# Performance work log

Measured on AMD Instinct MI355X. Metric: run time of the kernel, lower is better.

## Reference

```python
import jax, jax.numpy as jnp
import numpy as np

N, C = 20000, 512          # num_nodes, in_channels
E_RAND = 140000            # random edges (plus N self loops appended)
B, D = 128, 2              # num_bundles, bundle_dim
T = C // (B * D)           # feature cols per bundle (=2)
GNN_DIM = 512
NBP = B * (D * (D - 1) // 2)  # num_bun_params = 128 (1 angle per bundle since D=2)
MAX_DEG = 4
TAU = 1.0
EPS = 1e-5                 # BatchNorm1d eps


def setup_inputs() -> dict:
    key = jax.random.key(0)
    ks = jax.random.split(key, 8)
    x = jax.random.normal(ks[0], (N, C), jnp.float32)
    # edges: random + self-loops so every node has positive out-degree (finite deg_inv)
    src = jax.random.randint(ks[1], (E_RAND,), 0, N)
    dst = jax.random.randint(ks[2], (E_RAND,), 0, N)
    loop = jnp.arange(N)
    edge_index = jnp.stack([jnp.concatenate([src, loop]),
                            jnp.concatenate([dst, loop])]).astype(jnp.int64)
    s = 0.02
    W1 = jax.random.normal(ks[3], (C, GNN_DIM), jnp.float32) * s   # struct_enc lin1
    b1 = jnp.zeros((GNN_DIM,), jnp.float32)
    W2 = jax.random.normal(ks[4], (GNN_DIM, NBP), jnp.float32) * s # struct_enc lin2
    b2 = jnp.zeros((NBP,), jnp.float32)
    Wlin = jax.random.normal(ks[5], (C, C), jnp.float32) * s       # BuNNConv.lin
    blin = jnp.zeros((C,), jnp.float32)
    gamma = jnp.ones((C,), jnp.float32)                            # BatchNorm weight
    beta = jnp.zeros((C,), jnp.float32)                            # BatchNorm bias
    return dict(x=x, W1=W1, b1=b1, W2=W2, b2=b2, Wlin=Wlin, blin=blin,
                gamma=gamma, beta=beta, edge_index=edge_index)


def reference(x, W1, b1, W2, b2, Wlin, blin, gamma, beta, edge_index):
    src, dst = edge_index[0], edge_index[1]
    # degree of edge_index[0]; edge_weight = deg_inv[row] with row = edge_index[1]
    deg = jax.ops.segment_sum(jnp.ones_like(src, jnp.float32), src, num_segments=N)
    ew = (1.0 / deg)[dst]                                   # [E]

    # struct encoder (num_gnn == 0 branch): Linear -> GELU -> Linear -> 1 angle/bundle
    theta = jax.nn.gelu(x @ W1 + b1, approximate=False) @ W2 + b2   # [N, B]
    c, s = jnp.cos(theta), jnp.sin(theta)
    R = jnp.stack([jnp.stack([c, -s], -1),
                   jnp.stack([s, c], -1)], -2)              # [N, B, 2, 2] orthogonal

    # map into bundle frame
    vf = x.reshape(N, B, D, T)
    vf = jnp.einsum('nbij,nbjt->nbit', R, vf)
    h = vf.reshape(N, C)

    # truncated heat-kernel diffusion via scatter message passing
    cur = h
    for k in range(1, MAX_DEG + 1):
        agg = jax.ops.segment_sum(ew[:, None] * cur[src], dst, num_segments=N)
        cur = (-TAU / k) * (cur - agg)
        h = h + cur

    h = h @ Wlin + blin

    # map back with R^T
    vf = h.reshape(N, B, D, T)
    vf = jnp.einsum('nbji,nbjt->nbit', R, vf)
    h = vf.reshape(N, C)

    h = x + h                                # residual (dropout p = 0.0)
    mean = h.mean(axis=0)                    # BatchNorm1d, training mode, biased var
    var = h.var(axis=0)
    return (h - mean) / jnp.sqrt(var + EPS) * gamma + beta
```

## Files before the change

kernel.cpp:

```cpp
#include <hip/hip_runtime.h>

#define CC   512
#define BB_  128
#define BM 64
#define BN 128
#define BK 32

typedef __attribute__((ext_vector_type(8))) short short8;
typedef __attribute__((ext_vector_type(8))) unsigned short u16x8;
typedef __attribute__((ext_vector_type(4))) float f32x4;
typedef __attribute__((ext_vector_type(2))) float f32x2;
typedef __attribute__((ext_vector_type(4))) unsigned short u16x4;

__device__ __forceinline__ unsigned short f2bf(float f) {
  union { float f; unsigned u; } v; v.f = f;
  return (unsigned short)((v.u + 0x7FFFu + ((v.u >> 16) & 1u)) >> 16);
}
__device__ __forceinline__ float bf2f(unsigned short b) {
  union { unsigned u; float f; } v; v.u = ((unsigned)b) << 16;
  return v.f;
}

__device__ __forceinline__ void gload_lds16(const unsigned short* g, unsigned short* l) {
  __builtin_amdgcn_global_load_lds(
      (const __attribute__((address_space(1))) void*)g,
      (__attribute__((address_space(3))) void*)l, 16, 0, 0);
}

__global__ void k_zero(int* __restrict__ a, int* __restrict__ b, int* __restrict__ c,
                       float* __restrict__ d, float* __restrict__ e, int n) {
  int i = blockIdx.x * blockDim.x + threadIdx.x;
  if (i < n) { a[i] = 0; b[i] = 0; c[i] = 0; }
  if (i < CC) { d[i] = 0.f; e[i] = 0.f; }
}

__global__ void k_count(const int* __restrict__ src, const int* __restrict__ dst,
                        int* __restrict__ cnt_src, int* __restrict__ cnt_dst, int E) {
  int e = blockIdx.x * blockDim.x + threadIdx.x;
  if (e < E) {
    atomicAdd(&cnt_src[src[e]], 1);
    atomicAdd(&cnt_dst[dst[e]], 1);
  }
}

__global__ __launch_bounds__(1024) void k_scan(const int* __restrict__ cnt,
                                               const int* __restrict__ cnt_src,
                                               int* __restrict__ rp,
                                               float* __restrict__ dinv, int n) {
  __shared__ int sm[1024];
  int tid = threadIdx.x;
  for (int i = tid; i < n; i += 1024) dinv[i] = 1.0f / (float)cnt_src[i];
  int chunk = (n + 1023) >> 10;
  int beg = tid * chunk;
  int end = beg + chunk; if (end > n) end = n;
  int s = 0;
  for (int i = beg; i < end && i < n; ++i) s += cnt[i];
  sm[tid] = s;
  __syncthreads();
  for (int off = 1; off < 1024; off <<= 1) {
    int v = (tid >= off) ? sm[tid - off] : 0;
    __syncthreads();
    sm[tid] += v;
    __syncthreads();
  }
  int run = (tid == 0) ? 0 : sm[tid - 1];
  for (int i = beg; i < end && i < n; ++i) { rp[i] = run; run += cnt[i]; }
  if (tid == 0) rp[n] = sm[1023];
}

__global__ void k_fill(const int* __restrict__ src, const int* __restrict__ dst,
                       const int* __restrict__ rp, int* __restrict__ fil,
                       int* __restrict__ col, int E) {
  int e = blockIdx.x * blockDim.x + threadIdx.x;
  if (e < E) {
    int d = dst[e];
    int p = atomicAdd(&fil[d], 1);
    col[rp[d] + p] = src[e];
  }
}

__global__ void k_conv_bf16(const float* __restrict__ in, unsigned short* __restrict__ out,
                            int validRows, int total4) {
  int i4 = blockIdx.x * blockDim.x + threadIdx.x;
  if (i4 >= total4) return;
  int row = i4 / (CC / 4);
  u16x4 o;
  if (row < validRows) {
    f32x4 v = ((const f32x4*)in)[i4];
    o[0] = f2bf(v[0]); o[1] = f2bf(v[1]); o[2] = f2bf(v[2]); o[3] = f2bf(v[3]);
  } else {
    o[0] = 0; o[1] = 0; o[2] = 0; o[3] = 0;
  }
  ((u16x4*)out)[i4] = o;
}

__global__ void k_transconv(const float* __restrict__ W, unsigned short* __restrict__ Wt,
                            int K, int Nw) {
  __shared__ float tile[32][33];
  int n0 = blockIdx.x * 32, k0 = blockIdx.y * 32;
  int tx = threadIdx.x, ty = threadIdx.y;
  for (int j = 0; j < 4; ++j)
    tile[ty + j * 8][tx] = W[(k0 + ty + j * 8) * Nw + n0 + tx];
  __syncthreads();
  for (int j = 0; j < 4; ++j)
    Wt[(n0 + ty + j * 8) * K + k0 + tx] = f2bf(tile[tx][ty + j * 8]);
}

template <int EPI>
__device__ __forceinline__ void epi_store(float v, int row, int colL, void* outp,
                                          const float* x, unsigned short* c0,
                                          int Nw, int nvalid) {
  if (EPI == 0) {
    ((float*)outp)[(size_t)row * Nw + colL] = v;
  } else if (EPI == 1) {
    float g = 0.5f * v * (1.0f + erff(v * 0.70710678118654752f));
    ((unsigned short*)outp)[(size_t)row * Nw + colL] = f2bf(g);
  } else {
    size_t bidx = (size_t)row * Nw + colL;
    if (row < nvalid) {
      float sv, cv;
      sincosf(v, &sv, &cv);
      f32x2 o; o[0] = cv; o[1] = sv;
      ((f32x2*)outp)[bidx] = o;
      f32x4 xv = ((const f32x4*)x)[bidx];
      u16x4 rr;
      rr[0] = f2bf(cv * xv[0] - sv * xv[2]);
      rr[1] = f2bf(cv * xv[1] - sv * xv[3]);
      rr[2] = f2bf(sv * xv[0] + cv * xv[2]);
      rr[3] = f2bf(sv * xv[1] + cv * xv[3]);
      ((u16x4*)c0)[bidx] = rr;
    } else {
      u16x4 rr; rr[0] = 0; rr[1] = 0; rr[2] = 0; rr[3] = 0;
      ((u16x4*)c0)[bidx] = rr;
    }
  }
}

template <int EPI>
__global__ __launch_bounds__(256) void k_gemm(const unsigned short* __restrict__ A,
                                              const unsigned short* __restrict__ Bt,
                                              const float* __restrict__ bias,
                                              void* __restrict__ outp,
                                              const float* __restrict__ x,
                                              unsigned short* __restrict__ c0,
                                              int K, int Nw, int nvalid) {
  __shared__ unsigned short As[2][BM * BK];
  __shared__ unsigned short Bs[2][BN * BK];
  const int m0 = blockIdx.x * BM;
  const int n0 = blockIdx.y * BN;
  const int tid = threadIdx.x;
  const int wid = tid >> 6, lane = tid & 63;
  const int wr = wid >> 1, wc = wid & 1;
  const int l15 = lane & 15, kg = lane >> 4;
  const int arow = wid * 16 + (lane >> 2);
  const int aseg = (lane & 3) * 8;

  f32x4 acc00 = {}, acc01 = {}, acc02 = {}, acc03 = {};
  f32x4 acc10 = {}, acc11 = {}, acc12 = {}, acc13 = {};

  const int nt = K / BK;
  gload_lds16(&A[(size_t)(m0 + arow) * K + aseg],       &As[0][wid * 512]);
  gload_lds16(&Bt[(size_t)(n0 + arow) * K + aseg],      &Bs[0][wid * 512]);
  gload_lds16(&Bt[(size_t)(n0 + 64 + arow) * K + aseg], &Bs[0][2048 + wid * 512]);
  __syncthreads();

  for (int kk = 0; kk < nt; ++kk) {
    const int cur = kk & 1;
    if (kk + 1 < nt) {
      const int kt = (kk + 1) * BK;
      gload_lds16(&A[(size_t)(m0 + arow) * K + kt + aseg],       &As[cur ^ 1][wid * 512]);
      gload_lds16(&Bt[(size_t)(n0 + arow) * K + kt + aseg],      &Bs[cur ^ 1][wid * 512]);
      gload_lds16(&Bt[(size_t)(n0 + 64 + arow) * K + kt + aseg], &Bs[cur ^ 1][2048 + wid * 512]);
    }
    short8 af0 = *(const short8*)&As[cur][(wr * 32 +  0 + l15) * BK + kg * 8];
    short8 af1 = *(const short8*)&As[cur][(wr * 32 + 16 + l15) * BK + kg * 8];
    short8 bg0 = *(const short8*)&Bs[cur][(wc * 64 +  0 + l15) * BK + kg * 8];
    short8 bg1 = *(const short8*)&Bs[cur][(wc * 64 + 16 + l15) * BK + kg * 8];
    short8 bg2 = *(const short8*)&Bs[cur][(wc * 64 + 32 + l15) * BK + kg * 8];
    short8 bg3 = *(const short8*)&Bs[cur][(wc * 64 + 48 + l15) * BK + kg * 8];
    acc00 = __builtin_amdgcn_mfma_f32_16x16x32_bf16(af0, bg0, acc00, 0, 0, 0);
    acc01 = __builtin_amdgcn_mfma_f32_16x16x32_bf16(af0, bg1, acc01, 0, 0, 0);
    acc02 = __builtin_amdgcn_mfma_f32_16x16x32_bf16(af0, bg2, acc02, 0, 0, 0);
    acc03 = __builtin_amdgcn_mfma_f32_16x16x32_bf16(af0, bg3, acc03, 0, 0, 0);
    acc10 = __builtin_amdgcn_mfma_f32_16x16x32_bf16(af1, bg0, acc10, 0, 0, 0);
    acc11 = __builtin_amdgcn_mfma_f32_16x16x32_bf16(af1, bg1, acc11, 0, 0, 0);
    acc12 = __builtin_amdgcn_mfma_f32_16x16x32_bf16(af1, bg2, acc12, 0, 0, 0);
    acc13 = __builtin_amdgcn_mfma_f32_16x16x32_bf16(af1, bg3, acc13, 0, 0, 0);
    __syncthreads();
  }

#define DO_EPI(ACC, MI, NI)                                                     \
  do {                                                                          \
    const int row_ = m0 + wr * 32 + (MI) * 16 + kg * 4;                         \
    const int col_ = n0 + wc * 64 + (NI) * 16 + l15;                            \
    const float b_ = bias[col_];                                                \
    epi_store<EPI>(ACC[0] + b_, row_ + 0, col_, outp, x, c0, Nw, nvalid);       \
    epi_store<EPI>(ACC[1] + b_, row_ + 1, col_, outp, x, c0, Nw, nvalid);       \
    epi_store<EPI>(ACC[2] + b_, row_ + 2, col_, outp, x, c0, Nw, nvalid);       \
    epi_store<EPI>(ACC[3] + b_, row_ + 3, col_, outp, x, c0, Nw, nvalid);       \
  } while (0)

  DO_EPI(acc00, 0, 0); DO_EPI(acc01, 0, 1); DO_EPI(acc02, 0, 2); DO_EPI(acc03, 0, 3);
  DO_EPI(acc10, 1, 0); DO_EPI(acc11, 1, 1); DO_EPI(acc12, 1, 2); DO_EPI(acc13, 1, 3);
#undef DO_EPI
}

__global__ __launch_bounds__(256) void k_diffuse(const unsigned short* __restrict__ cur,
                                                 unsigned short* __restrict__ nxt,
                                                 const float* __restrict__ dinv,
                                                 const int* __restrict__ rp,
                                                 const int* __restrict__ col,
                                                 float coef, int n) {
  int w = threadIdx.x >> 6, lane = threadIdx.x & 63;
  int v = blockIdx.x * 4 + w;
  if (v >= n) return;
  int beg = rp[v], end = rp[v + 1];
  const u16x8* curv = (const u16x8*)cur;
  float s[8] = {0.f,0.f,0.f,0.f,0.f,0.f,0.f,0.f};
  for (int e = beg; e < end; ++e) {
    int u = col[e];
    u16x8 r = curv[(size_t)u * 64 + lane];
    #pragma unroll
    for (int j = 0; j < 8; ++j) s[j] += bf2f(r[j]);
  }
  float di = dinv[v];
  u16x8 cv = curv[(size_t)v * 64 + lane];
  u16x8 o;
  #pragma unroll
  for (int j = 0; j < 8; ++j) o[j] = f2bf((bf2f(cv[j]) - s[j] * di) * coef);
  ((u16x8*)nxt)[(size_t)v * 64 + lane] = o;
}

__global__ __launch_bounds__(256) void k_diffuse_final(const unsigned short* __restrict__ c0,
                                                       const unsigned short* __restrict__ c1,
                                                       const unsigned short* __restrict__ c2,
                                                       const unsigned short* __restrict__ cur,
                                                       unsigned short* __restrict__ hb,
                                                       const float* __restrict__ dinv,
                                                       const int* __restrict__ rp,
                                                       const int* __restrict__ col,
                                                       float coef, int n) {
  int w = threadIdx.x >> 6, lane = threadIdx.x & 63;
  int v = blockIdx.x * 4 + w;
  if (v >= n) return;
  int beg = rp[v], end = rp[v + 1];
  const u16x8* curv = (const u16x8*)cur;
  float s[8] = {0.f,0.f,0.f,0.f,0.f,0.f,0.f,0.f};
  for (int e = beg; e < end; ++e) {
    int u = col[e];
    u16x8 r = curv[(size_t)u * 64 + lane];
    #pragma unroll
    for (int j = 0; j < 8; ++j) s[j] += bf2f(r[j]);
  }
  float di = dinv[v];
  size_t o = (size_t)v * 64 + lane;
  u16x8 cv = curv[o];
  u16x8 a0 = ((const u16x8*)c0)[o];
  u16x8 a1 = ((const u16x8*)c1)[o];
  u16x8 a2 = ((const u16x8*)c2)[o];
  u16x8 hv;
  #pragma unroll
  for (int j = 0; j < 8; ++j) {
    float c3v = bf2f(cv[j]);
    float c4v = (c3v - s[j] * di) * coef;
    hv[j] = f2bf(bf2f(a0[j]) + bf2f(a1[j]) + bf2f(a2[j]) + c3v + c4v);
  }
  ((u16x8*)hb)[o] = hv;
}

__global__ __launch_bounds__(256) void k_rotback_stats(const float* __restrict__ x,
                                                       const f32x2* __restrict__ cs,
                                                       const float* __restrict__ h2,
                                                       float* __restrict__ out,
                                                       float* __restrict__ colsum,
                                                       float* __restrict__ colsq,
                                                       int nb) {
  __shared__ float ssum[CC], ssq[CC];
  int t = threadIdx.x;
  for (int c = t; c < CC; c += 256) { ssum[c] = 0.f; ssq[c] = 0.f; }
  __syncthreads();
  int cg = ((blockIdx.x << 8) + t) & (BB_ - 1);
  float ls0 = 0.f, ls1 = 0.f, ls2 = 0.f, ls3 = 0.f;
  float lq0 = 0.f, lq1 = 0.f, lq2 = 0.f, lq3 = 0.f;
  for (int idx = (blockIdx.x << 8) + t; idx < nb; idx += gridDim.x << 8) {
    f32x2 a = cs[idx];
    float c = a[0], s = a[1];
    f32x4 v = ((const f32x4*)h2)[idx];
    f32x4 xx = ((const f32x4*)x)[idx];
    f32x4 o;
    o[0] = xx[0] + c * v[0] + s * v[2];
    o[1] = xx[1] + c * v[1] + s * v[3];
    o[2] = xx[2] - s * v[0] + c * v[2];
    o[3] = xx[3] - s * v[1] + c * v[3];
    ((f32x4*)out)[idx] = o;
    ls0 += o[0]; lq0 += o[0] * o[0];
    ls1 += o[1]; lq1 += o[1] * o[1];
    ls2 += o[2]; lq2 += o[2] * o[2];
    ls3 += o[3]; lq3 += o[3] * o[3];
  }
  atomicAdd(&ssum[cg * 4 + 0], ls0); atomicAdd(&ssq[cg * 4 + 0], lq0);
  atomicAdd(&ssum[cg * 4 + 1], ls1); atomicAdd(&ssq[cg * 4 + 1], lq1);
  atomicAdd(&ssum[cg * 4 + 2], ls2); atomicAdd(&ssq[cg * 4 + 2], lq2);
  atomicAdd(&ssum[cg * 4 + 3], ls3); atomicAdd(&ssq[cg * 4 + 3], lq3);
  __syncthreads();
  for (int c = t; c < CC; c += 256) {
    atomicAdd(&colsum[c], ssum[c]);
    atomicAdd(&colsq[c], ssq[c]);
  }
}

__global__ void k_bnfinal(const float* __restrict__ sum, const float* __restrict__ sumsq,
                          const float* __restrict__ gamma, const float* __restrict__ beta,
                          float* __restrict__ scale, float* __restrict__ shift, int n) {
  int c = threadIdx.x;
  float inv = 1.0f / (float)n;
  float mean = sum[c] * inv;
  float var = sumsq[c] * inv - mean * mean;
  float sc = gamma[c] * rsqrtf(var + 1e-5f);
  scale[c] = sc;
  shift[c] = beta[c] - mean * sc;
}

__global__ void k_norm(float* __restrict__ out, const float* __restrict__ scale,
                       const float* __restrict__ shift, int n4) {
  int i = blockIdx.x * blockDim.x + threadIdx.x;
  if (i >= n4) return;
  int c4 = i & (CC / 4 - 1);
  f32x4 v = ((f32x4*)out)[i];
  f32x4 sc = ((const f32x4*)scale)[c4];
  f32x4 sh = ((const f32x4*)shift)[c4];
  ((f32x4*)out)[i] = v * sc + sh;
}

extern "C" void kernel_launch(void* const* d_in, const int* in_sizes, int n_in,
                              void* d_out, int out_size, void* d_ws, size_t ws_size,
                              hipStream_t stream) {
  (void)n_in; (void)out_size; (void)ws_size;
  const float* x    = (const float*)d_in[0];
  const float* W1   = (const float*)d_in[1];
  const float* b1   = (const float*)d_in[2];
  const float* W2   = (const float*)d_in[3];
  const float* b2   = (const float*)d_in[4];
  const float* Wlin = (const float*)d_in[5];
  const float* blin = (const float*)d_in[6];
  const float* gamma = (const float*)d_in[7];
  const float* beta  = (const float*)d_in[8];
  const int*   ei    = (const int*)d_in[9];

  const int n   = in_sizes[0] / CC;
  const int E   = in_sizes[9] / 2;
  const int GNN = in_sizes[2];
  const int NBP = in_sizes[4];
  const int* src = ei;
  const int* dst = ei + E;
  const int mt64 = (n + BM - 1) / BM;
  const int mpad = 20096;
  const size_t SB = (size_t)mpad * CC;

  char* ws = (char*)d_ws;
  size_t off = 0;
  auto alloc = [&](size_t bytes) -> void* {
    void* p = ws + off;
    off = (off + bytes + 255) & ~(size_t)255;
    return p;
  };
  int*   cnt_src = (int*)alloc((size_t)n * 4);
  int*   cnt_dst = (int*)alloc((size_t)n * 4);
  int*   fil     = (int*)alloc((size_t)n * 4);
  int*   rp      = (int*)alloc((size_t)(n + 1) * 4);
  int*   colx    = (int*)alloc((size_t)E * 4);
  float* dinv    = (float*)alloc((size_t)n * 4);
  float* colsum  = (float*)alloc(CC * 4);
  float* colsq   = (float*)alloc(CC * 4);
  float* scale   = (float*)alloc(CC * 4);
  float* shift   = (float*)alloc(CC * 4);
  unsigned short* W1t = (unsigned short*)alloc((size_t)GNN * CC * 2);
  unsigned short* W2t = (unsigned short*)alloc((size_t)NBP * GNN * 2);
  unsigned short* Wlt = (unsigned short*)alloc((size_t)CC * CC * 2);
  f32x2* cs = (f32x2*)alloc((size_t)mpad * BB_ * 8);
  unsigned short* c0   = (unsigned short*)alloc(SB * 2);
  unsigned short* c1   = (unsigned short*)alloc(SB * 2);
  unsigned short* slab = (unsigned short*)alloc(SB * 2 * 3);
  unsigned short* c2 = slab;
  unsigned short* c3 = slab + SB;
  unsigned short* hb = slab + 2 * SB;
  unsigned short* xb = c0;
  unsigned short* G  = c1;
  float* OUT3 = (float*)slab;

  k_zero<<<(n + 255) / 256, 256, 0, stream>>>(cnt_src, cnt_dst, fil, colsum, colsq, n);

  k_count<<<(E + 255) / 256, 256, 0, stream>>>(src, dst, cnt_src, cnt_dst, E);
  k_scan<<<1, 1024, 0, stream>>>(cnt_dst, cnt_src, rp, dinv, n);
  k_fill<<<(E + 255) / 256, 256, 0, stream>>>(src, dst, rp, fil, colx, E);

  int total4 = mpad * (CC / 4);
  k_conv_bf16<<<(total4 + 255) / 256, 256, 0, stream>>>(x, xb, n, total4);
  dim3 tb(32, 8);
  k_transconv<<<dim3(GNN / 32, CC / 32), tb, 0, stream>>>(W1, W1t, CC, GNN);
  k_transconv<<<dim3(NBP / 32, GNN / 32), tb, 0, stream>>>(W2, W2t, GNN, NBP);
  k_transconv<<<dim3(CC / 32, CC / 32), tb, 0, stream>>>(Wlin, Wlt, CC, CC);

  k_gemm<1><<<dim3(mt64, GNN / BN), 256, 0, stream>>>(xb, W1t, b1, (void*)G, nullptr, nullptr, CC, GNN, n);
  k_gemm<2><<<dim3(mt64, NBP / BN), 256, 0, stream>>>(G, W2t, b2, (void*)cs, x, c0, GNN, NBP, n);

  float coef1 = -1.0f, coef2 = -0.5f, coef3 = -1.0f / 3.0f, coef4 = -0.25f;
  k_diffuse<<<(n + 3) / 4, 256, 0, stream>>>(c0, c1, dinv, rp, colx, coef1, n);
  k_diffuse<<<(n + 3) / 4, 256, 0, stream>>>(c1, c2, dinv, rp, colx, coef2, n);
  k_diffuse<<<(n + 3) / 4, 256, 0, stream>>>(c2, c3, dinv, rp, colx, coef3, n);
  k_diffuse_final<<<(n + 3) / 4, 256, 0, stream>>>(c0, c1, c2, c3, hb, dinv, rp, colx, coef4, n);

  k_gemm<0><<<dim3(mt64, CC / BN), 256, 0, stream>>>(hb, Wlt, blin, (void*)OUT3, nullptr, nullptr, CC, CC, n);

  int nb = n * BB_;
  k_rotback_stats<<<512, 256, 0, stream>>>(x, cs, OUT3, (float*)d_out, colsum, colsq, nb);
  k_bnfinal<<<1, 512, 0, stream>>>(colsum, colsq, gamma, beta, scale, shift, n);
  k_norm<<<(nb + 255) / 256, 256, 0, stream>>>((float*)d_out, scale, shift, nb);
}
```

Baseline: 330.6 us.

## Merge diffusion passes into one cooperative kernel and fold small launches

```diff
diff --git a/kernel.cpp b/kernel.cpp
--- a/kernel.cpp
+++ b/kernel.cpp
@@ -1,4 +1,7 @@
 #include <hip/hip_runtime.h>
+#include <hip/hip_cooperative_groups.h>
+
+namespace cg = cooperative_groups;
 
 #define CC   512
 #define BB_  128
@@ -44,12 +47,9 @@
 }
 
 __global__ __launch_bounds__(1024) void k_scan(const int* __restrict__ cnt,
-                                               const int* __restrict__ cnt_src,
-                                               int* __restrict__ rp,
-                                               float* __restrict__ dinv, int n) {
+                                               int* __restrict__ rp, int n) {
   __shared__ int sm[1024];
   int tid = threadIdx.x;
-  for (int i = tid; i < n; i += 1024) dinv[i] = 1.0f / (float)cnt_src[i];
   int chunk = (n + 1023) >> 10;
   int beg = tid * chunk;
   int end = beg + chunk; if (end > n) end = n;
@@ -94,8 +94,14 @@
   ((u16x4*)out)[i4] = o;
 }
 
-__global__ void k_transconv(const float* __restrict__ W, unsigned short* __restrict__ Wt,
-                            int K, int Nw) {
+__global__ void k_transconv_all(const float* __restrict__ W1, const float* __restrict__ W2,
+                                const float* __restrict__ Wlin,
+                                unsigned short* __restrict__ W1t, unsigned short* __restrict__ W2t,
+                                unsigned short* __restrict__ Wlt) {
+  const float* W; unsigned short* Wt; int K, Nw;
+  if (blockIdx.z == 0)      { W = W1;   Wt = W1t; K = 512; Nw = 512; }
+  else if (blockIdx.z == 1) { W = W2;   Wt = W2t; K = 512; Nw = 128; if (blockIdx.x >= 4) return; }
+  else                      { W = Wlin; Wt = Wlt; K = 512; Nw = 512; }
   __shared__ float tile[32][33];
   int n0 = blockIdx.x * 32, k0 = blockIdx.y * 32;
   int tx = threadIdx.x, ty = threadIdx.y;
@@ -205,67 +211,71 @@
 #undef DO_EPI
 }
 
-__global__ __launch_bounds__(256) void k_diffuse(const unsigned short* __restrict__ cur,
-                                                 unsigned short* __restrict__ nxt,
-                                                 const float* __restrict__ dinv,
-                                                 const int* __restrict__ rp,
-                                                 const int* __restrict__ col,
-                                                 float coef, int n) {
-  int w = threadIdx.x >> 6, lane = threadIdx.x & 63;
-  int v = blockIdx.x * 4 + w;
-  if (v >= n) return;
-  int beg = rp[v], end = rp[v + 1];
-  const u16x8* curv = (const u16x8*)cur;
-  float s[8] = {0.f,0.f,0.f,0.f,0.f,0.f,0.f,0.f};
-  for (int e = beg; e < end; ++e) {
-    int u = col[e];
-    u16x8 r = curv[(size_t)u * 64 + lane];
+__global__ __launch_bounds__(256) void k_diffuse_all(const unsigned short* __restrict__ c0,
+                                                     unsigned short* __restrict__ c1,
+                                                     unsigned short* __restrict__ c2,
+                                                     unsigned short* __restrict__ c3,
+                                                     unsigned short* __restrict__ hb,
+                                                     const int* __restrict__ cnt_src,
+                                                     const int* __restrict__ rp,
+                                                     const int* __restrict__ col,
+                                                     int n) {
+  cg::grid_group grid = cg::this_grid();
+  const int nw = (gridDim.x * 256) >> 6;
+  const int w = (blockIdx.x * 256 + threadIdx.x) >> 6;
+  const int lane = threadIdx.x & 63;
+
+#define DIFF_PASS(SRC, DST, COEF)                                              \
+  for (int v = w; v < n; v += nw) {                                            \
+    int beg = rp[v], end = rp[v + 1];                                          \
+    const u16x8* curv = (const u16x8*)(SRC);                                   \
+    float s[8] = {0.f,0.f,0.f,0.f,0.f,0.f,0.f,0.f};                            \
+    for (int e = beg; e < end; ++e) {                                          \
+      int u = col[e];                                                          \
+      u16x8 r = curv[(size_t)u * 64 + lane];                                   \
+      _Pragma("unroll")                                                        \
+      for (int j = 0; j < 8; ++j) s[j] += bf2f(r[j]);                          \
+    }                                                                          \
+    float di = 1.0f / (float)cnt_src[v];                                       \
+    size_t o = (size_t)v * 64 + lane;                                          \
+    u16x8 cv = curv[o];                                                        \
+    u16x8 ov;                                                                  \
+    _Pragma("unroll")                                                          \
+    for (int j = 0; j < 8; ++j) ov[j] = f2bf((bf2f(cv[j]) - s[j] * di) * (COEF)); \
+    ((u16x8*)(DST))[o] = ov;                                                   \
+  }                                                                            \
+  grid.sync();
+
+  DIFF_PASS(c0, c1, -1.0f)
+  DIFF_PASS(c1, c2, -0.5f)
+  DIFF_PASS(c2, c3, -(1.0f / 3.0f))
+#undef DIFF_PASS
+
+  for (int v = w; v < n; v += nw) {
+    int beg = rp[v], end = rp[v + 1];
+    const u16x8* curv = (const u16x8*)c3;
+    float s[8] = {0.f,0.f,0.f,0.f,0.f,0.f,0.f,0.f};
+    for (int e = beg; e < end; ++e) {
+      int u = col[e];
+      u16x8 r = curv[(size_t)u * 64 + lane];
+      #pragma unroll
+      for (int j = 0; j < 8; ++j) s[j] += bf2f(r[j]);
+    }
+    float di = 1.0f / (float)cnt_src[v];
+    size_t o = (size_t)v * 64 + lane;
+    u16x8 cv = curv[o];
+    u16x8 a0 = ((const u16x8*)c0)[o];
+    u16x8 a1 = ((const u16x8*)c1)[o];
+    u16x8 a2 = ((const u16x8*)c2)[o];
+    u16x8 hv;
     #pragma unroll
-    for (int j = 0; j < 8; ++j) s[j] += bf2f(r[j]);
-  }
-  float di = dinv[v];
-  u16x8 cv = curv[(size_t)v * 64 + lane];
-  u16x8 o;
-  #pragma unroll
-  for (int j = 0; j < 8; ++j) o[j] = f2bf((bf2f(cv[j]) - s[j] * di) * coef);
-  ((u16x8*)nxt)[(size_t)v * 64 + lane] = o;
-}
-
-__global__ __launch_bounds__(256) void k_diffuse_final(const unsigned short* __restrict__ c0,
-                                                       const unsigned short* __restrict__ c1,
-                                                       const unsigned short* __restrict__ c2,
-                                                       const unsigned short* __restrict__ cur,
-                                                       unsigned short* __restrict__ hb,
-                                                       const float* __restrict__ dinv,
-                                                       const int* __restrict__ rp,
-                                                       const int* __restrict__ col,
-                                                       float coef, int n) {
-  int w = threadIdx.x >> 6, lane = threadIdx.x & 63;
-  int v = blockIdx.x * 4 + w;
-  if (v >= n) return;
-  int beg = rp[v], end = rp[v + 1];
-  const u16x8* curv = (const u16x8*)cur;
-  float s[8] = {0.f,0.f,0.f,0.f,0.f,0.f,0.f,0.f};
-  for (int e = beg; e < end; ++e) {
-    int u = col[e];
-    u16x8 r = curv[(size_t)u * 64 + lane];
-    #pragma unroll
-    for (int j = 0; j < 8; ++j) s[j] += bf2f(r[j]);
-  }
-  float di = dinv[v];
-  size_t o = (size_t)v * 64 + lane;
-  u16x8 cv = curv[o];
-  u16x8 a0 = ((const u16x8*)c0)[o];
-  u16x8 a1 = ((const u16x8*)c1)[o];
-  u16x8 a2 = ((const u16x8*)c2)[o];
-  u16x8 hv;
-  #pragma unroll
-  for (int j = 0; j < 8; ++j) {
-    float c3v = bf2f(cv[j]);
-    float c4v = (c3v - s[j] * di) * coef;
-    hv[j] = f2bf(bf2f(a0[j]) + bf2f(a1[j]) + bf2f(a2[j]) + c3v + c4v);
-  }
-  ((u16x8*)hb)[o] = hv;
+    for (int j = 0; j < 8; ++j) {
+      float c3v = bf2f(cv[j]);
+      float c4v = (c3v - s[j] * di) * -0.25f;
+      hv[j] = f2bf(bf2f(a0[j]) + bf2f(a1[j]) + bf2f(a2[j]) + c3v + c4v);
+    }
+    ((u16x8*)hb)[o] = hv;
+  }
 }
 
 __global__ __launch_bounds__(256) void k_rotback_stats(const float* __restrict__ x,
@@ -279,7 +289,7 @@
   int t = threadIdx.x;
   for (int c = t; c < CC; c += 256) { ssum[c] = 0.f; ssq[c] = 0.f; }
   __syncthreads();
-  int cg = ((blockIdx.x << 8) + t) & (BB_ - 1);
+  int cg_ = ((blockIdx.x << 8) + t) & (BB_ - 1);
   float ls0 = 0.f, ls1 = 0.f, ls2 = 0.f, ls3 = 0.f;
   float lq0 = 0.f, lq1 = 0.f, lq2 = 0.f, lq3 = 0.f;
   for (int idx = (blockIdx.x << 8) + t; idx < nb; idx += gridDim.x << 8) {
@@ -298,10 +308,10 @@
     ls2 += o[2]; lq2 += o[2] * o[2];
     ls3 += o[3]; lq3 += o[3] * o[3];
   }
-  atomicAdd(&ssum[cg * 4 + 0], ls0); atomicAdd(&ssq[cg * 4 + 0], lq0);
-  atomicAdd(&ssum[cg * 4 + 1], ls1); atomicAdd(&ssq[cg * 4 + 1], lq1);
-  atomicAdd(&ssum[cg * 4 + 2], ls2); atomicAdd(&ssq[cg * 4 + 2], lq2);
-  atomicAdd(&ssum[cg * 4 + 3], ls3); atomicAdd(&ssq[cg * 4 + 3], lq3);
+  atomicAdd(&ssum[cg_ * 4 + 0], ls0); atomicAdd(&ssq[cg_ * 4 + 0], lq0);
+  atomicAdd(&ssum[cg_ * 4 + 1], ls1); atomicAdd(&ssq[cg_ * 4 + 1], lq1);
+  atomicAdd(&ssum[cg_ * 4 + 2], ls2); atomicAdd(&ssq[cg_ * 4 + 2], lq2);
+  atomicAdd(&ssum[cg_ * 4 + 3], ls3); atomicAdd(&ssq[cg_ * 4 + 3], lq3);
   __syncthreads();
   for (int c = t; c < CC; c += 256) {
     atomicAdd(&colsum[c], ssum[c]);
@@ -309,26 +319,28 @@
   }
 }
 
-__global__ void k_bnfinal(const float* __restrict__ sum, const float* __restrict__ sumsq,
-                          const float* __restrict__ gamma, const float* __restrict__ beta,
-                          float* __restrict__ scale, float* __restrict__ shift, int n) {
-  int c = threadIdx.x;
-  float inv = 1.0f / (float)n;
-  float mean = sum[c] * inv;
-  float var = sumsq[c] * inv - mean * mean;
-  float sc = gamma[c] * rsqrtf(var + 1e-5f);
-  scale[c] = sc;
-  shift[c] = beta[c] - mean * sc;
-}
-
-__global__ void k_norm(float* __restrict__ out, const float* __restrict__ scale,
-                       const float* __restrict__ shift, int n4) {
-  int i = blockIdx.x * blockDim.x + threadIdx.x;
+__global__ __launch_bounds__(256) void k_norm(float* __restrict__ out,
+                                              const float* __restrict__ colsum,
+                                              const float* __restrict__ colsq,
+                                              const float* __restrict__ gamma,
+                                              const float* __restrict__ beta,
+                                              float invn, int n4) {
+  __shared__ float ssc[CC], ssh[CC];
+  int t = threadIdx.x;
+  for (int c = t; c < CC; c += 256) {
+    float mean = colsum[c] * invn;
+    float var = colsq[c] * invn - mean * mean;
+    float sc = gamma[c] * rsqrtf(var + 1e-5f);
+    ssc[c] = sc;
+    ssh[c] = beta[c] - mean * sc;
+  }
+  __syncthreads();
+  int i = blockIdx.x * blockDim.x + t;
   if (i >= n4) return;
   int c4 = i & (CC / 4 - 1);
   f32x4 v = ((f32x4*)out)[i];
-  f32x4 sc = ((const f32x4*)scale)[c4];
-  f32x4 sh = ((const f32x4*)shift)[c4];
+  f32x4 sc = *(const f32x4*)&ssc[c4 * 4];
+  f32x4 sh = *(const f32x4*)&ssh[c4 * 4];
   ((f32x4*)out)[i] = v * sc + sh;
 }
 
@@ -369,11 +381,8 @@
   int*   fil     = (int*)alloc((size_t)n * 4);
   int*   rp      = (int*)alloc((size_t)(n + 1) * 4);
   int*   colx    = (int*)alloc((size_t)E * 4);
-  float* dinv    = (float*)alloc((size_t)n * 4);
   float* colsum  = (float*)alloc(CC * 4);
   float* colsq   = (float*)alloc(CC * 4);
-  float* scale   = (float*)alloc(CC * 4);
-  float* shift   = (float*)alloc(CC * 4);
   unsigned short* W1t = (unsigned short*)alloc((size_t)GNN * CC * 2);
   unsigned short* W2t = (unsigned short*)alloc((size_t)NBP * GNN * 2);
   unsigned short* Wlt = (unsigned short*)alloc((size_t)CC * CC * 2);
@@ -391,29 +400,27 @@
   k_zero<<<(n + 255) / 256, 256, 0, stream>>>(cnt_src, cnt_dst, fil, colsum, colsq, n);
 
   k_count<<<(E + 255) / 256, 256, 0, stream>>>(src, dst, cnt_src, cnt_dst, E);
-  k_scan<<<1, 1024, 0, stream>>>(cnt_dst, cnt_src, rp, dinv, n);
+  k_scan<<<1, 1024, 0, stream>>>(cnt_dst, rp, n);
   k_fill<<<(E + 255) / 256, 256, 0, stream>>>(src, dst, rp, fil, colx, E);
 
   int total4 = mpad * (CC / 4);
   k_conv_bf16<<<(total4 + 255) / 256, 256, 0, stream>>>(x, xb, n, total4);
-  dim3 tb(32, 8);
-  k_transconv<<<dim3(GNN / 32, CC / 32), tb, 0, stream>>>(W1, W1t, CC, GNN);
-  k_transconv<<<dim3(NBP / 32, GNN / 32), tb, 0, stream>>>(W2, W2t, GNN, NBP);
-  k_transconv<<<dim3(CC / 32, CC / 32), tb, 0, stream>>>(Wlin, Wlt, CC, CC);
+  k_transconv_all<<<dim3(16, 16, 3), dim3(32, 8), 0, stream>>>(W1, W2, Wlin, W1t, W2t, Wlt);
 
   k_gemm<1><<<dim3(mt64, GNN / BN), 256, 0, stream>>>(xb, W1t, b1, (void*)G, nullptr, nullptr, CC, GNN, n);
   k_gemm<2><<<dim3(mt64, NBP / BN), 256, 0, stream>>>(G, W2t, b2, (void*)cs, x, c0, GNN, NBP, n);
 
-  float coef1 = -1.0f, coef2 = -0.5f, coef3 = -1.0f / 3.0f, coef4 = -0.25f;
-  k_diffuse<<<(n + 3) / 4, 256, 0, stream>>>(c0, c1, dinv, rp, colx, coef1, n);
-  k_diffuse<<<(n + 3) / 4, 256, 0, stream>>>(c1, c2, dinv, rp, colx, coef2, n);
-  k_diffuse<<<(n + 3) / 4, 256, 0, stream>>>(c2, c3, dinv, rp, colx, coef3, n);
-  k_diffuse_final<<<(n + 3) / 4, 256, 0, stream>>>(c0, c1, c2, c3, hb, dinv, rp, colx, coef4, n);
+  {
+    int nn = n;
+    void* dargs[] = {(void*)&c0, (void*)&c1, (void*)&c2, (void*)&c3, (void*)&hb,
+                     (void*)&cnt_src, (void*)&rp, (void*)&colx, (void*)&nn};
+    hipLaunchCooperativeKernel((void*)k_diffuse_all, dim3(1024), dim3(256), dargs, 0, stream);
+  }
 
   k_gemm<0><<<dim3(mt64, CC / BN), 256, 0, stream>>>(hb, Wlt, blin, (void*)OUT3, nullptr, nullptr, CC, CC, n);
 
   int nb = n * BB_;
   k_rotback_stats<<<512, 256, 0, stream>>>(x, cs, OUT3, (float*)d_out, colsum, colsq, nb);
-  k_bnfinal<<<1, 512, 0, stream>>>(colsum, colsq, gamma, beta, scale, shift, n);
-  k_norm<<<(nb + 255) / 256, 256, 0, stream>>>((float*)d_out, scale, shift, nb);
-}
+  k_norm<<<(nb + 255) / 256, 256, 0, stream>>>((float*)d_out, colsum, colsq, gamma, beta,
+                                               1.0f / (float)n, nb);
+}
```

Measured after the change: 747.6 us. +126.1%, slower.

## Fuse rotate-back, residual and BN stats into final GEMM epilogue; merge small kernels

Applied to the files above, without the earlier changes.

```diff
diff --git a/kernel.cpp b/kernel.cpp
--- a/kernel.cpp
+++ b/kernel.cpp
@@ -44,12 +44,9 @@
 }
 
 __global__ __launch_bounds__(1024) void k_scan(const int* __restrict__ cnt,
-                                               const int* __restrict__ cnt_src,
-                                               int* __restrict__ rp,
-                                               float* __restrict__ dinv, int n) {
+                                               int* __restrict__ rp, int n) {
   __shared__ int sm[1024];
   int tid = threadIdx.x;
-  for (int i = tid; i < n; i += 1024) dinv[i] = 1.0f / (float)cnt_src[i];
   int chunk = (n + 1023) >> 10;
   int beg = tid * chunk;
   int end = beg + chunk; if (end > n) end = n;
@@ -94,8 +91,14 @@
   ((u16x4*)out)[i4] = o;
 }
 
-__global__ void k_transconv(const float* __restrict__ W, unsigned short* __restrict__ Wt,
-                            int K, int Nw) {
+__global__ void k_transconv_all(const float* __restrict__ W1, const float* __restrict__ W2,
+                                const float* __restrict__ Wlin,
+                                unsigned short* __restrict__ W1t, unsigned short* __restrict__ W2t,
+                                unsigned short* __restrict__ Wlt) {
+  const float* W; unsigned short* Wt; int K, Nw;
+  if (blockIdx.z == 0)      { W = W1;   Wt = W1t; K = 512; Nw = 512; }
+  else if (blockIdx.z == 1) { W = W2;   Wt = W2t; K = 512; Nw = 128; if (blockIdx.x >= 4) return; }
+  else                      { W = Wlin; Wt = Wlt; K = 512; Nw = 512; }
   __shared__ float tile[32][33];
   int n0 = blockIdx.x * 32, k0 = blockIdx.y * 32;
   int tx = threadIdx.x, ty = threadIdx.y;
@@ -143,9 +146,13 @@
                                               void* __restrict__ outp,
                                               const float* __restrict__ x,
                                               unsigned short* __restrict__ c0,
+                                              const f32x2* __restrict__ csr,
+                                              float* __restrict__ csum,
+                                              float* __restrict__ csq,
                                               int K, int Nw, int nvalid) {
   __shared__ unsigned short As[2][BM * BK];
   __shared__ unsigned short Bs[2][BN * BK];
+  __shared__ float s_sum[BN], s_sq[BN];
   const int m0 = blockIdx.x * BM;
   const int n0 = blockIdx.y * BN;
   const int tid = threadIdx.x;
@@ -154,6 +161,8 @@
   const int l15 = lane & 15, kg = lane >> 4;
   const int arow = wid * 16 + (lane >> 2);
   const int aseg = (lane & 3) * 8;
+
+  if (EPI == 3 && tid < BN) { s_sum[tid] = 0.f; s_sq[tid] = 0.f; }
 
   f32x4 acc00 = {}, acc01 = {}, acc02 = {}, acc03 = {};
   f32x4 acc10 = {}, acc11 = {}, acc12 = {}, acc13 = {};
@@ -189,6 +198,7 @@
     __syncthreads();
   }
 
+  if (EPI != 3) {
 #define DO_EPI(ACC, MI, NI)                                                     \
   do {                                                                          \
     const int row_ = m0 + wr * 32 + (MI) * 16 + kg * 4;                         \
@@ -200,14 +210,54 @@
     epi_store<EPI>(ACC[3] + b_, row_ + 3, col_, outp, x, c0, Nw, nvalid);       \
   } while (0)
 
-  DO_EPI(acc00, 0, 0); DO_EPI(acc01, 0, 1); DO_EPI(acc02, 0, 2); DO_EPI(acc03, 0, 3);
-  DO_EPI(acc10, 1, 0); DO_EPI(acc11, 1, 1); DO_EPI(acc12, 1, 2); DO_EPI(acc13, 1, 3);
+    DO_EPI(acc00, 0, 0); DO_EPI(acc01, 0, 1); DO_EPI(acc02, 0, 2); DO_EPI(acc03, 0, 3);
+    DO_EPI(acc10, 1, 0); DO_EPI(acc11, 1, 1); DO_EPI(acc12, 1, 2); DO_EPI(acc13, 1, 3);
 #undef DO_EPI
+  } else {
+    float pS0 = 0.f, pS1 = 0.f, pS2 = 0.f, pS3 = 0.f;
+    float pQ0 = 0.f, pQ1 = 0.f, pQ2 = 0.f, pQ3 = 0.f;
+    const int bi = (l15 >> 1) & 1;
+#define DO_EPI3(ACC, MI, NI, PS, PQ)                                            \
+  do {                                                                          \
+    const int row_ = m0 + wr * 32 + (MI) * 16 + kg * 4;                         \
+    const int col_ = n0 + wc * 64 + (NI) * 16 + l15;                            \
+    const float b_ = bias[col_];                                                \
+    _Pragma("unroll")                                                           \
+    for (int r = 0; r < 4; ++r) {                                               \
+      float v = ACC[r] + b_;                                                    \
+      float vp = __shfl_xor(v, 2);           \
+      int rr_ = row_ + r;                                                       \
+      if (rr_ < nvalid) {                                                       \
+        f32x2 a = csr[(size_t)rr_ * BB_ + (col_ >> 2)];                         \
+        float ov = bi == 0 ? a[0] * v + a[1] * vp : a[0] * v - a[1] * vp;       \
+        ov += x[(size_t)rr_ * CC + col_];                                       \
+        ((float*)outp)[(size_t)rr_ * CC + col_] = ov;                           \
+        PS += ov; PQ += ov * ov;                                                \
+      }                                                                         \
+    }                                                                           \
+  } while (0)
+
+    DO_EPI3(acc00, 0, 0, pS0, pQ0); DO_EPI3(acc01, 0, 1, pS1, pQ1);
+    DO_EPI3(acc02, 0, 2, pS2, pQ2); DO_EPI3(acc03, 0, 3, pS3, pQ3);
+    DO_EPI3(acc10, 1, 0, pS0, pQ0); DO_EPI3(acc11, 1, 1, pS1, pQ1);
+    DO_EPI3(acc12, 1, 2, pS2, pQ2); DO_EPI3(acc13, 1, 3, pS3, pQ3);
+#undef DO_EPI3
+    const int cb = wc * 64 + l15;
+    atomicAdd(&s_sum[cb +  0], pS0); atomicAdd(&s_sq[cb +  0], pQ0);
+    atomicAdd(&s_sum[cb + 16], pS1); atomicAdd(&s_sq[cb + 16], pQ1);
+    atomicAdd(&s_sum[cb + 32], pS2); atomicAdd(&s_sq[cb + 32], pQ2);
+    atomicAdd(&s_sum[cb + 48], pS3); atomicAdd(&s_sq[cb + 48], pQ3);
+    __syncthreads();
+    if (tid < BN) {
+      atomicAdd(&csum[n0 + tid], s_sum[tid]);
+      atomicAdd(&csq[n0 + tid], s_sq[tid]);
+    }
+  }
 }
 
 __global__ __launch_bounds__(256) void k_diffuse(const unsigned short* __restrict__ cur,
                                                  unsigned short* __restrict__ nxt,
-                                                 const float* __restrict__ dinv,
+                                                 const int* __restrict__ cnt_src,
                                                  const int* __restrict__ rp,
                                                  const int* __restrict__ col,
                                                  float coef, int n) {
@@ -223,7 +273,7 @@
     #pragma unroll
     for (int j = 0; j < 8; ++j) s[j] += bf2f(r[j]);
   }
-  float di = dinv[v];
+  float di = 1.0f / (float)cnt_src[v];
   u16x8 cv = curv[(size_t)v * 64 + lane];
   u16x8 o;
   #pragma unroll
@@ -236,7 +286,7 @@
                                                        const unsigned short* __restrict__ c2,
                                                        const unsigned short* __restrict__ cur,
                                                        unsigned short* __restrict__ hb,
-                                                       const float* __restrict__ dinv,
+                                                       const int* __restrict__ cnt_src,
                                                        const int* __restrict__ rp,
                                                        const int* __restrict__ col,
                                                        float coef, int n) {
@@ -252,7 +302,7 @@
     #pragma unroll
     for (int j = 0; j < 8; ++j) s[j] += bf2f(r[j]);
   }
-  float di = dinv[v];
+  float di = 1.0f / (float)cnt_src[v];
   size_t o = (size_t)v * 64 + lane;
   u16x8 cv = curv[o];
   u16x8 a0 = ((const u16x8*)c0)[o];
@@ -268,67 +318,28 @@
   ((u16x8*)hb)[o] = hv;
 }
 
-__global__ __launch_bounds__(256) void k_rotback_stats(const float* __restrict__ x,
-                                                       const f32x2* __restrict__ cs,
-                                                       const float* __restrict__ h2,
-                                                       float* __restrict__ out,
-                                                       float* __restrict__ colsum,
-                                                       float* __restrict__ colsq,
-                                                       int nb) {
-  __shared__ float ssum[CC], ssq[CC];
+__global__ __launch_bounds__(256) void k_norm(float* __restrict__ out,
+                                              const float* __restrict__ colsum,
+                                              const float* __restrict__ colsq,
+                                              const float* __restrict__ gamma,
+                                              const float* __restrict__ beta,
+                                              float invn, int n4) {
+  __shared__ float ssc[CC], ssh[CC];
   int t = threadIdx.x;
-  for (int c = t; c < CC; c += 256) { ssum[c] = 0.f; ssq[c] = 0.f; }
+  for (int c = t; c < CC; c += 256) {
+    float mean = colsum[c] * invn;
+    float var = colsq[c] * invn - mean * mean;
+    float sc = gamma[c] * rsqrtf(var + 1e-5f);
+    ssc[c] = sc;
+    ssh[c] = beta[c] - mean * sc;
+  }
   __syncthreads();
-  int cg = ((blockIdx.x << 8) + t) & (BB_ - 1);
-  float ls0 = 0.f, ls1 = 0.f, ls2 = 0.f, ls3 = 0.f;
-  float lq0 = 0.f, lq1 = 0.f, lq2 = 0.f, lq3 = 0.f;
-  for (int idx = (blockIdx.x << 8) + t; idx < nb; idx += gridDim.x << 8) {
-    f32x2 a = cs[idx];
-    float c = a[0], s = a[1];
-    f32x4 v = ((const f32x4*)h2)[idx];
-    f32x4 xx = ((const f32x4*)x)[idx];
-    f32x4 o;
-    o[0] = xx[0] + c * v[0] + s * v[2];
-    o[1] = xx[1] + c * v[1] + s * v[3];
-    o[2] = xx[2] - s * v[0] + c * v[2];
-    o[3] = xx[3] - s * v[1] + c * v[3];
-    ((f32x4*)out)[idx] = o;
-    ls0 += o[0]; lq0 += o[0] * o[0];
-    ls1 += o[1]; lq1 += o[1] * o[1];
-    ls2 += o[2]; lq2 += o[2] * o[2];
-    ls3 += o[3]; lq3 += o[3] * o[3];
-  }
-  atomicAdd(&ssum[cg * 4 + 0], ls0); atomicAdd(&ssq[cg * 4 + 0], lq0);
-  atomicAdd(&ssum[cg * 4 + 1], ls1); atomicAdd(&ssq[cg * 4 + 1], lq1);
-  atomicAdd(&ssum[cg * 4 + 2], ls2); atomicAdd(&ssq[cg * 4 + 2], lq2);
-  atomicAdd(&ssum[cg * 4 + 3], ls3); atomicAdd(&ssq[cg * 4 + 3], lq3);
-  __syncthreads();
-  for (int c = t; c < CC; c += 256) {
-    atomicAdd(&colsum[c], ssum[c]);
-    atomicAdd(&colsq[c], ssq[c]);
-  }
-}
-
-__global__ void k_bnfinal(const float* __restrict__ sum, const float* __restrict__ sumsq,
-                          const float* __restrict__ gamma, const float* __restrict__ beta,
-                          float* __restrict__ scale, float* __restrict__ shift, int n) {
-  int c = threadIdx.x;
-  float inv = 1.0f / (float)n;
-  float mean = sum[c] * inv;
-  float var = sumsq[c] * inv - mean * mean;
-  float sc = gamma[c] * rsqrtf(var + 1e-5f);
-  scale[c] = sc;
-  shift[c] = beta[c] - mean * sc;
-}
-
-__global__ void k_norm(float* __restrict__ out, const float* __restrict__ scale,
-                       const float* __restrict__ shift, int n4) {
-  int i = blockIdx.x * blockDim.x + threadIdx.x;
+  int i = blockIdx.x * blockDim.x + t;
   if (i >= n4) return;
   int c4 = i & (CC / 4 - 1);
   f32x4 v = ((f32x4*)out)[i];
-  f32x4 sc = ((const f32x4*)scale)[c4];
-  f32x4 sh = ((const f32x4*)shift)[c4];
+  f32x4 sc = *(const f32x4*)&ssc[c4 * 4];
+  f32x4 sh = *(const f32x4*)&ssh[c4 * 4];
   ((f32x4*)out)[i] = v * sc + sh;
 }
 
@@ -369,51 +380,44 @@
   int*   fil     = (int*)alloc((size_t)n * 4);
   int*   rp      = (int*)alloc((size_t)(n + 1) * 4);
   int*   colx    = (int*)alloc((size_t)E * 4);
-  float* dinv    = (float*)alloc((size_t)n * 4);
   float* colsum  = (float*)alloc(CC * 4);
   float* colsq   = (float*)alloc(CC * 4);
-  float* scale   = (float*)alloc(CC * 4);
-  float* shift   = (float*)alloc(CC * 4);
   unsigned short* W1t = (unsigned short*)alloc((size_t)GNN * CC * 2);
   unsigned short* W2t = (unsigned short*)alloc((size_t)NBP * GNN * 2);
   unsigned short* Wlt = (unsigned short*)alloc((size_t)CC * CC * 2);
   f32x2* cs = (f32x2*)alloc((size_t)mpad * BB_ * 8);
-  unsigned short* c0   = (unsigned short*)alloc(SB * 2);
-  unsigned short* c1   = (unsigned short*)alloc(SB * 2);
-  unsigned short* slab = (unsigned short*)alloc(SB * 2 * 3);
-  unsigned short* c2 = slab;
-  unsigned short* c3 = slab + SB;
-  unsigned short* hb = slab + 2 * SB;
+  unsigned short* c0 = (unsigned short*)alloc(SB * 2);
+  unsigned short* c1 = (unsigned short*)alloc(SB * 2);
+  unsigned short* c2 = (unsigned short*)alloc(SB * 2);
+  unsigned short* c3 = (unsigned short*)alloc(SB * 2);
+  unsigned short* hb = (unsigned short*)alloc(SB * 2);
   unsigned short* xb = c0;
   unsigned short* G  = c1;
-  float* OUT3 = (float*)slab;
 
   k_zero<<<(n + 255) / 256, 256, 0, stream>>>(cnt_src, cnt_dst, fil, colsum, colsq, n);
 
   k_count<<<(E + 255) / 256, 256, 0, stream>>>(src, dst, cnt_src, cnt_dst, E);
-  k_scan<<<1, 1024, 0, stream>>>(cnt_dst, cnt_src, rp, dinv, n);
+  k_scan<<<1, 1024, 0, stream>>>(cnt_dst, rp, n);
   k_fill<<<(E + 255) / 256, 256, 0, stream>>>(src, dst, rp, fil, colx, E);
 
   int total4 = mpad * (CC / 4);
   k_conv_bf16<<<(total4 + 255) / 256, 256, 0, stream>>>(x, xb, n, total4);
-  dim3 tb(32, 8);
-  k_transconv<<<dim3(GNN / 32, CC / 32), tb, 0, stream>>>(W1, W1t, CC, GNN);
-  k_transconv<<<dim3(NBP / 32, GNN / 32), tb, 0, stream>>>(W2, W2t, GNN, NBP);
-  k_transconv<<<dim3(CC / 32, CC / 32), tb, 0, stream>>>(Wlin, Wlt, CC, CC);
-
-  k_gemm<1><<<dim3(mt64, GNN / BN), 256, 0, stream>>>(xb, W1t, b1, (void*)G, nullptr, nullptr, CC, GNN, n);
-  k_gemm<2><<<dim3(mt64, NBP / BN), 256, 0, stream>>>(G, W2t, b2, (void*)cs, x, c0, GNN, NBP, n);
-
-  float coef1 = -1.0f, coef2 = -0.5f, coef3 = -1.0f / 3.0f, coef4 = -0.25f;
-  k_diffuse<<<(n + 3) / 4, 256, 0, stream>>>(c0, c1, dinv, rp, colx, coef1, n);
-  k_diffuse<<<(n + 3) / 4, 256, 0, stream>>>(c1, c2, dinv, rp, colx, coef2, n);
-  k_diffuse<<<(n + 3) / 4, 256, 0, stream>>>(c2, c3, dinv, rp, colx, coef3, n);
-  k_diffuse_final<<<(n + 3) / 4, 256, 0, stream>>>(c0, c1, c2, c3, hb, dinv, rp, colx, coef4, n);
-
-  k_gemm<0><<<dim3(mt64, CC / BN), 256, 0, stream>>>(hb, Wlt, blin, (void*)OUT3, nullptr, nullptr, CC, CC, n);
+  k_transconv_all<<<dim3(16, 16, 3), dim3(32, 8), 0, stream>>>(W1, W2, Wlin, W1t, W2t, Wlt);
+
+  k_gemm<1><<<dim3(mt64, GNN / BN), 256, 0, stream>>>(xb, W1t, b1, (void*)G, nullptr, nullptr,
+                                                      nullptr, nullptr, nullptr, CC, GNN, n);
+  k_gemm<2><<<dim3(mt64, NBP / BN), 256, 0, stream>>>(G, W2t, b2, (void*)cs, x, c0,
+                                                      nullptr, nullptr, nullptr, GNN, NBP, n);
+
+  k_diffuse<<<(n + 3) / 4, 256, 0, stream>>>(c0, c1, cnt_src, rp, colx, -1.0f, n);
+  k_diffuse<<<(n + 3) / 4, 256, 0, stream>>>(c1, c2, cnt_src, rp, colx, -0.5f, n);
+  k_diffuse<<<(n + 3) / 4, 256, 0, stream>>>(c2, c3, cnt_src, rp, colx, -(1.0f / 3.0f), n);
+  k_diffuse_final<<<(n + 3) / 4, 256, 0, stream>>>(c0, c1, c2, c3, hb, cnt_src, rp, colx, -0.25f, n);
+
+  k_gemm<3><<<dim3(mt64, CC / BN), 256, 0, stream>>>(hb, Wlt, blin, d_out, x, nullptr,
+                                                     cs, colsum, colsq, CC, CC, n);
 
   int nb = n * BB_;
-  k_rotback_stats<<<512, 256, 0, stream>>>(x, cs, OUT3, (float*)d_out, colsum, colsq, nb);
-  k_bnfinal<<<1, 512, 0, stream>>>(colsum, colsq, gamma, beta, scale, shift, n);
-  k_norm<<<(nb + 255) / 256, 256, 0, stream>>>((float*)d_out, scale, shift, nb);
-}
+  k_norm<<<(nb + 255) / 256, 256, 0, stream>>>((float*)d_out, colsum, colsq, gamma, beta,
+                                               1.0f / (float)n, nb);
+}
```

New measurement: 319.7 us. 1.03x faster.
